# Kernel tuning notes

Measured on AMD Instinct MI355X. Metric: run time of the kernel, lower is better.

The kernel has to match this reference:

```python
import jax, jax.numpy as jnp
import numpy as np

B, V, NF, H, W, K = 16, 6890, 13776, 512, 512, 1
SIGMA = 1e-4   # BlendParams default
GAMMA = 1e-4   # BlendParams default
ZNEAR, ZFAR = 1.0, 100.0  # softmax_rgb_blend defaults (cameras not forwarded)
BG = jnp.zeros((3,), jnp.float32)  # background_color = 0.0
EPS = 1e-10


def setup_inputs() -> dict:
    key = jax.random.key(0)
    k0, k1, k2, k3, k4 = jax.random.split(key, 5)
    mesh_verts = jax.random.normal(k0, (B, V, 3), jnp.float32)
    mesh_faces = jax.random.randint(k1, (NF, 3), 0, V)
    pix_to_face = jax.random.randint(k2, (B, H, W, K), -1, NF)  # -1 = background
    zbuf = jax.random.uniform(k3, (B, H, W, K), jnp.float32, 0.0, 100.0)
    dists = jax.random.normal(k4, (B, H, W, K), jnp.float32) * SIGMA
    return {"mesh_verts": mesh_verts, "zbuf": zbuf, "dists": dists,
            "mesh_faces": mesh_faces, "pix_to_face": pix_to_face}


def _vertex_normals(verts, faces):
    # pytorch3d Meshes.verts_normals: area-weighted face normals scattered to verts
    fv = verts[:, faces]                                   # [B, F, 3(verts), 3(xyz)]
    fn = jnp.cross(fv[:, :, 1] - fv[:, :, 0], fv[:, :, 2] - fv[:, :, 0])  # [B,F,3]
    vn = jnp.zeros_like(verts)
    vn = vn.at[:, faces[:, 0]].add(fn)
    vn = vn.at[:, faces[:, 1]].add(fn)
    vn = vn.at[:, faces[:, 2]].add(fn)
    nrm = jnp.linalg.norm(vn, axis=-1, keepdims=True)
    return vn / jnp.maximum(nrm, 1e-6)                     # F.normalize(eps=1e-6)


def reference(mesh_verts, zbuf, dists, mesh_faces, pix_to_face):
    vn = _vertex_normals(mesh_verts, mesh_faces)           # [B, V, 3]
    # interpolate_face_attributes with bary = ones -> sum of the face's 3 vertex normals
    face_attr_sum = vn[:, mesh_faces].sum(axis=2)          # [B, F, 3]
    idx = jnp.clip(pix_to_face, 0, NF - 1)                 # [B, H, W, K]
    pn = jax.vmap(lambda t, i: t[i])(face_attr_sum, idx)   # [B, H, W, K, 3]
    valid = (pix_to_face >= 0)                             # [B, H, W, K]
    pn = pn * valid[..., None].astype(pn.dtype)
    # F.normalize(dim=-1), torch eps=1e-12 via clamp_min on the norm
    pn_nrm = jnp.linalg.norm(pn, axis=-1, keepdims=True)
    pixel_normals = pn / jnp.maximum(pn_nrm, 1e-12)        # [B, H, W, K, 3]

    # softmax_rgb_blend (colors = pixel_normals)
    maskf = valid.astype(jnp.float32)
    prob = jax.nn.sigmoid(-dists / SIGMA) * maskf          # [B, H, W, K]
    alpha = 1.0 - jnp.prod(1.0 - prob, axis=-1)            # [B, H, W]
    z_inv = (ZFAR - zbuf) / (ZFAR - ZNEAR) * maskf
    z_inv_max = jnp.maximum(jnp.max(z_inv, axis=-1, keepdims=True), EPS)
    weights_num = prob * jnp.exp((z_inv - z_inv_max) / GAMMA)
    delta = jnp.maximum(jnp.exp((EPS - z_inv_max) / GAMMA), EPS)
    denom = weights_num.sum(axis=-1, keepdims=True) + delta
    weighted_colors = jnp.einsum('bhwk,bhwkc->bhwc', weights_num / denom, pixel_normals)
    weighted_bg = (delta / denom) * BG                     # [B, H, W, 3]
    rendered_rgb = weighted_colors + weighted_bg
    rendered_alpha = (1.0 - alpha)[..., None]              # [B, H, W, 1]

    # faces_per_pixel == 1 path: mask from norm of (normalized) pixel normals
    hit = jnp.linalg.norm(pixel_normals, axis=-1) != 0     # [B, H, W, K]
    normalized_img = pixel_normals[:, :, :, 0, :] + (1.0 - hit[..., 0:1].astype(jnp.float32))
    out = jnp.concatenate([normalized_img, rendered_alpha], axis=-1)  # [B, H, W, 4]
    return out
```

## Files before the change

kernel.cpp:

```cpp
#include <hip/hip_runtime.h>
#include <math.h>

#define BB 16
#define VV 6890
#define NFF 13776
#define HH 512
#define WW 512

typedef float nf4 __attribute__((ext_vector_type(4)));

__global__ __launch_bounds__(256) void k_fn(const float* __restrict__ verts,
                                            const int* __restrict__ faces,
                                            float4* __restrict__ fn4) {
    int i = blockIdx.x * 256 + threadIdx.x;
    if (i >= BB * NFF) return;
    int b = i / NFF;
    int f = i - b * NFF;
    int i0 = faces[3 * f + 0];
    int i1 = faces[3 * f + 1];
    int i2 = faces[3 * f + 2];
    const float* vb = verts + (size_t)b * (VV * 3);
    float ax = vb[3 * i0 + 0], ay = vb[3 * i0 + 1], az = vb[3 * i0 + 2];
    float bx = vb[3 * i1 + 0], by = vb[3 * i1 + 1], bz = vb[3 * i1 + 2];
    float cx = vb[3 * i2 + 0], cy = vb[3 * i2 + 1], cz = vb[3 * i2 + 2];
    float e1x = bx - ax, e1y = by - ay, e1z = bz - az;
    float e2x = cx - ax, e2y = cy - ay, e2z = cz - az;
    float4 n;
    n.x = e1y * e2z - e1z * e2y;
    n.y = e1z * e2x - e1x * e2z;
    n.z = e1x * e2y - e1y * e2x;
    n.w = 0.f;
    fn4[i] = n;
}

__global__ __launch_bounds__(256) void k_count(const int* __restrict__ faces,
                                               int* __restrict__ counts) {
    int f = blockIdx.x * 256 + threadIdx.x;
    if (f >= NFF) return;
    atomicAdd(&counts[faces[3 * f + 0]], 1);
    atomicAdd(&counts[faces[3 * f + 1]], 1);
    atomicAdd(&counts[faces[3 * f + 2]], 1);
}

#define SCAN_T 1024
__global__ __launch_bounds__(SCAN_T) void k_scan(int* __restrict__ counts) {
    __shared__ int part[SCAN_T];
    const int CH = (VV + SCAN_T - 1) / SCAN_T;
    int t = threadIdx.x;
    int base = t * CH;
    int local = 0;
    for (int k = 0; k < CH; k++) {
        int idx = base + k;
        if (idx < VV) local += counts[idx];
    }
    part[t] = local;
    __syncthreads();
    for (int off = 1; off < SCAN_T; off <<= 1) {
        int v = part[t];
        int add = (t >= off) ? part[t - off] : 0;
        __syncthreads();
        part[t] = v + add;
        __syncthreads();
    }
    int running = (t == 0) ? 0 : part[t - 1];
    for (int k = 0; k < CH; k++) {
        int idx = base + k;
        if (idx < VV) {
            int c = counts[idx];
            counts[idx] = running;
            running += c;
        }
    }
    if (t == 0) counts[VV] = part[SCAN_T - 1];
}

__global__ __launch_bounds__(256) void k_fill(const int* __restrict__ faces,
                                              const int* __restrict__ offsets,
                                              int* __restrict__ cursor,
                                              int* __restrict__ adj) {
    int f = blockIdx.x * 256 + threadIdx.x;
    if (f >= NFF) return;
    for (int c = 0; c < 3; c++) {
        int v = faces[3 * f + c];
        int pos = offsets[v] + atomicAdd(&cursor[v], 1);
        adj[pos] = f;
    }
}

__global__ __launch_bounds__(256) void k_vn(const float4* __restrict__ fn4,
                                            const int* __restrict__ offsets,
                                            const int* __restrict__ adj,
                                            float4* __restrict__ vn4) {
    int i = blockIdx.x * 256 + threadIdx.x;
    if (i >= BB * VV) return;
    int b = i / VV;
    int v = i - b * VV;
    int s = offsets[v], e = offsets[v + 1];
    float x = 0.f, y = 0.f, z = 0.f;
    const float4* fnb = fn4 + (size_t)b * NFF;
    for (int j = s; j < e; j++) {
        float4 n = fnb[adj[j]];
        x += n.x; y += n.y; z += n.z;
    }
    float nrm = sqrtf(x * x + y * y + z * z);
    float inv = 1.0f / fmaxf(nrm, 1e-6f);
    float4 o; o.x = x * inv; o.y = y * inv; o.z = z * inv; o.w = 0.f;
    vn4[i] = o;
}

__global__ __launch_bounds__(256) void k_face_sum(const float4* __restrict__ vn4,
                                                  const int* __restrict__ faces,
                                                  float4* __restrict__ fas4) {
    int i = blockIdx.x * 256 + threadIdx.x;
    if (i >= BB * NFF) return;
    int b = i / NFF;
    int f = i - b * NFF;
    int i0 = faces[3 * f + 0], i1 = faces[3 * f + 1], i2 = faces[3 * f + 2];
    const float4* vnb = vn4 + (size_t)b * VV;
    float4 a = vnb[i0], bb = vnb[i1], cc = vnb[i2];
    float4 o;
    o.x = a.x + bb.x + cc.x;
    o.y = a.y + bb.y + cc.y;
    o.z = a.z + bb.z + cc.z;
    o.w = 0.f;
    fas4[i] = o;
}

__device__ __forceinline__ nf4 pixel_one(int f, float d, const float4* __restrict__ fasb) {
    float px = 0.f, py = 0.f, pz = 0.f, prob = 0.f;
    if (f >= 0) {
        int fc = f < (NFF - 1) ? f : (NFF - 1);
        float4 p = fasb[fc];
        px = p.x; py = p.y; pz = p.z;
        prob = 1.0f / (1.0f + __expf(d * 1.0e4f));
    }
    float n2 = px * px + py * py + pz * pz;
    float inv = 1.0f / fmaxf(sqrtf(n2), 1e-12f);
    float hitadd = (n2 > 0.f) ? 0.f : 1.0f;
    nf4 o;
    o.x = px * inv + hitadd;
    o.y = py * inv + hitadd;
    o.z = pz * inv + hitadd;
    o.w = 1.0f - prob;
    return o;
}

__global__ __launch_bounds__(256) void k_pixel(const int* __restrict__ p2f,
                                               const float* __restrict__ dists,
                                               const float4* __restrict__ fas4,
                                               nf4* __restrict__ out) {
    int i = (blockIdx.x * 256 + threadIdx.x) * 2;
    if (i >= BB * HH * WW) return;
    int b = i >> 18;
    int2 ff = *(const int2*)(p2f + i);
    float2 dd = *(const float2*)(dists + i);
    const float4* fasb = fas4 + (size_t)b * NFF;
    nf4 o0 = pixel_one(ff.x, dd.x, fasb);
    nf4 o1 = pixel_one(ff.y, dd.y, fasb);
    __builtin_nontemporal_store(o0, &out[i]);
    __builtin_nontemporal_store(o1, &out[i + 1]);
}

extern "C" void kernel_launch(void* const* d_in, const int* in_sizes, int n_in,
                              void* d_out, int out_size, void* d_ws, size_t ws_size,
                              hipStream_t stream) {
    const float* verts = (const float*)d_in[0];
    const float* dists = (const float*)d_in[2];
    const int* faces   = (const int*)d_in[3];
    const int* p2f     = (const int*)d_in[4];

    char* w = (char*)d_ws;
    float4* fn4  = (float4*)w;                         w += (size_t)BB * NFF * 16;
    float4* vn4  = (float4*)w;                         w += (size_t)BB * VV * 16;
    float4* fas4 = (float4*)w;                         w += (size_t)BB * NFF * 16;
    int* counts  = (int*)w;                            w += ((VV + 1) * 4 + 12) / 16 * 16;
    int* cursor  = (int*)w;                            w += (VV * 4 + 15) / 16 * 16;
    int* adj     = (int*)w;                            w += NFF * 3 * 4;

    (void)hipMemsetAsync(counts, 0, (size_t)((VV + 1) + VV) * sizeof(int) + 32, stream);

    int nbf = BB * NFF;
    int nbv = BB * VV;

    k_fn<<<(nbf + 255) / 256, 256, 0, stream>>>(verts, faces, fn4);
    k_count<<<(NFF + 255) / 256, 256, 0, stream>>>(faces, counts);
    k_scan<<<1, SCAN_T, 0, stream>>>(counts);
    k_fill<<<(NFF + 255) / 256, 256, 0, stream>>>(faces, counts, cursor, adj);
    k_vn<<<(nbv + 255) / 256, 256, 0, stream>>>(fn4, counts, adj, vn4);
    k_face_sum<<<(nbf + 255) / 256, 256, 0, stream>>>(vn4, faces, fas4);

    int npix = BB * HH * WW;
    k_pixel<<<npix / 2 / 256, 256, 0, stream>>>(p2f, dists, fas4, (nf4*)d_out);
}
```

Measured before the change: 175.5 us.

## Fuse adjacency build into one shared-memory block and widen pixel kernel

Replaces the separate face-normal, count, scan and fill kernels plus the memset with a single launch. Block 0 builds the vertex-to-face CSR adjacency in shared memory while the other blocks compute face normals, which removes several launch gaps and global atomics. The pixel kernel now handles 8 pixels per thread with vector loads, branchless masking and hardware reciprocal instructions. Block 0 serialises the whole histogram, scan and fill on one CU and could become the critical path, and rcpf is less precise than a true division.

```diff
diff --git a/kernel.cpp b/kernel.cpp
--- a/kernel.cpp
+++ b/kernel.cpp
@@ -8,82 +8,74 @@
 #define WW 512
 
 typedef float nf4 __attribute__((ext_vector_type(4)));
+typedef int   ni4 __attribute__((ext_vector_type(4)));
 
-__global__ __launch_bounds__(256) void k_fn(const float* __restrict__ verts,
-                                            const int* __restrict__ faces,
-                                            float4* __restrict__ fn4) {
-    int i = blockIdx.x * 256 + threadIdx.x;
-    if (i >= BB * NFF) return;
-    int b = i / NFF;
-    int f = i - b * NFF;
-    int i0 = faces[3 * f + 0];
-    int i1 = faces[3 * f + 1];
-    int i2 = faces[3 * f + 2];
-    const float* vb = verts + (size_t)b * (VV * 3);
-    float ax = vb[3 * i0 + 0], ay = vb[3 * i0 + 1], az = vb[3 * i0 + 2];
-    float bx = vb[3 * i1 + 0], by = vb[3 * i1 + 1], bz = vb[3 * i1 + 2];
-    float cx = vb[3 * i2 + 0], cy = vb[3 * i2 + 1], cz = vb[3 * i2 + 2];
-    float e1x = bx - ax, e1y = by - ay, e1z = bz - az;
-    float e2x = cx - ax, e2y = cy - ay, e2z = cz - az;
-    float4 n;
-    n.x = e1y * e2z - e1z * e2y;
-    n.y = e1z * e2x - e1x * e2z;
-    n.z = e1x * e2y - e1y * e2x;
-    n.w = 0.f;
-    fn4[i] = n;
-}
+#define GEOT 1024
 
-__global__ __launch_bounds__(256) void k_count(const int* __restrict__ faces,
-                                               int* __restrict__ counts) {
-    int f = blockIdx.x * 256 + threadIdx.x;
-    if (f >= NFF) return;
-    atomicAdd(&counts[faces[3 * f + 0]], 1);
-    atomicAdd(&counts[faces[3 * f + 1]], 1);
-    atomicAdd(&counts[faces[3 * f + 2]], 1);
-}
-
-#define SCAN_T 1024
-__global__ __launch_bounds__(SCAN_T) void k_scan(int* __restrict__ counts) {
-    __shared__ int part[SCAN_T];
-    const int CH = (VV + SCAN_T - 1) / SCAN_T;
-    int t = threadIdx.x;
-    int base = t * CH;
-    int local = 0;
-    for (int k = 0; k < CH; k++) {
-        int idx = base + k;
-        if (idx < VV) local += counts[idx];
-    }
-    part[t] = local;
-    __syncthreads();
-    for (int off = 1; off < SCAN_T; off <<= 1) {
-        int v = part[t];
-        int add = (t >= off) ? part[t - off] : 0;
+__global__ __launch_bounds__(GEOT) void k_geo(const float* __restrict__ verts,
+                                              const int* __restrict__ faces,
+                                              float4* __restrict__ fn4,
+                                              int* __restrict__ offsets,
+                                              int* __restrict__ adj) {
+    int blk = blockIdx.x;
+    if (blk == 0) {
+        __shared__ int hist[VV];
+        __shared__ int part[GEOT];
+        int t = threadIdx.x;
+        for (int v = t; v < VV; v += GEOT) hist[v] = 0;
         __syncthreads();
-        part[t] = v + add;
+        for (int e = t; e < NFF * 3; e += GEOT) atomicAdd(&hist[faces[e]], 1);
         __syncthreads();
-    }
-    int running = (t == 0) ? 0 : part[t - 1];
-    for (int k = 0; k < CH; k++) {
-        int idx = base + k;
-        if (idx < VV) {
-            int c = counts[idx];
-            counts[idx] = running;
-            running += c;
+        const int CH = (VV + GEOT - 1) / GEOT;
+        int base = t * CH;
+        int local = 0;
+        for (int k = 0; k < CH; k++) { int idx = base + k; if (idx < VV) local += hist[idx]; }
+        part[t] = local;
+        __syncthreads();
+        for (int off = 1; off < GEOT; off <<= 1) {
+            int v = part[t];
+            int add = (t >= off) ? part[t - off] : 0;
+            __syncthreads();
+            part[t] = v + add;
+            __syncthreads();
         }
-    }
-    if (t == 0) counts[VV] = part[SCAN_T - 1];
-}
-
-__global__ __launch_bounds__(256) void k_fill(const int* __restrict__ faces,
-                                              const int* __restrict__ offsets,
-                                              int* __restrict__ cursor,
-                                              int* __restrict__ adj) {
-    int f = blockIdx.x * 256 + threadIdx.x;
-    if (f >= NFF) return;
-    for (int c = 0; c < 3; c++) {
-        int v = faces[3 * f + c];
-        int pos = offsets[v] + atomicAdd(&cursor[v], 1);
-        adj[pos] = f;
+        int running = (t == 0) ? 0 : part[t - 1];
+        for (int k = 0; k < CH; k++) {
+            int idx = base + k;
+            if (idx < VV) {
+                int c = hist[idx];
+                hist[idx] = running;
+                offsets[idx] = running;
+                running += c;
+            }
+        }
+        if (t == 0) offsets[VV] = NFF * 3;
+        __syncthreads();
+        for (int e = t; e < NFF * 3; e += GEOT) {
+            int v = faces[e];
+            int pos = atomicAdd(&hist[v], 1);
+            adj[pos] = e / 3;
+        }
+    } else {
+        int i = (blk - 1) * GEOT + threadIdx.x;
+        if (i >= BB * NFF) return;
+        int b = i / NFF;
+        int f = i - b * NFF;
+        int i0 = faces[3 * f + 0];
+        int i1 = faces[3 * f + 1];
+        int i2 = faces[3 * f + 2];
+        const float* vb = verts + (size_t)b * (VV * 3);
+        float ax = vb[3 * i0 + 0], ay = vb[3 * i0 + 1], az = vb[3 * i0 + 2];
+        float bx = vb[3 * i1 + 0], by = vb[3 * i1 + 1], bz = vb[3 * i1 + 2];
+        float cx = vb[3 * i2 + 0], cy = vb[3 * i2 + 1], cz = vb[3 * i2 + 2];
+        float e1x = bx - ax, e1y = by - ay, e1z = bz - az;
+        float e2x = cx - ax, e2y = cy - ay, e2z = cz - az;
+        float4 n;
+        n.x = e1y * e2z - e1z * e2y;
+        n.y = e1z * e2x - e1x * e2z;
+        n.z = e1x * e2y - e1y * e2x;
+        n.w = 0.f;
+        fn4[i] = n;
     }
 }
 
@@ -102,8 +94,7 @@
         float4 n = fnb[adj[j]];
         x += n.x; y += n.y; z += n.z;
     }
-    float nrm = sqrtf(x * x + y * y + z * z);
-    float inv = 1.0f / fmaxf(nrm, 1e-6f);
+    float inv = 1.0f / fmaxf(sqrtf(x * x + y * y + z * z), 1e-6f);
     float4 o; o.x = x * inv; o.y = y * inv; o.z = z * inv; o.w = 0.f;
     vn4[i] = o;
 }
@@ -127,15 +118,13 @@
 }
 
 __device__ __forceinline__ nf4 pixel_one(int f, float d, const float4* __restrict__ fasb) {
-    float px = 0.f, py = 0.f, pz = 0.f, prob = 0.f;
-    if (f >= 0) {
-        int fc = f < (NFF - 1) ? f : (NFF - 1);
-        float4 p = fasb[fc];
-        px = p.x; py = p.y; pz = p.z;
-        prob = 1.0f / (1.0f + __expf(d * 1.0e4f));
-    }
+    int fc = f < 0 ? 0 : (f < (NFF - 1) ? f : (NFF - 1));
+    float m = (f >= 0) ? 1.0f : 0.0f;
+    float4 p = fasb[fc];
+    float px = p.x * m, py = p.y * m, pz = p.z * m;
+    float prob = m * __builtin_amdgcn_rcpf(1.0f + __expf(d * 1.0e4f));
     float n2 = px * px + py * py + pz * pz;
-    float inv = 1.0f / fmaxf(sqrtf(n2), 1e-12f);
+    float inv = __builtin_amdgcn_rcpf(fmaxf(sqrtf(n2), 1e-12f));
     float hitadd = (n2 > 0.f) ? 0.f : 1.0f;
     nf4 o;
     o.x = px * inv + hitadd;
@@ -149,16 +138,30 @@
                                                const float* __restrict__ dists,
                                                const float4* __restrict__ fas4,
                                                nf4* __restrict__ out) {
-    int i = (blockIdx.x * 256 + threadIdx.x) * 2;
+    int i = (blockIdx.x * 256 + threadIdx.x) * 8;
     if (i >= BB * HH * WW) return;
     int b = i >> 18;
-    int2 ff = *(const int2*)(p2f + i);
-    float2 dd = *(const float2*)(dists + i);
+    ni4 f0 = *(const ni4*)(p2f + i);
+    ni4 f1 = *(const ni4*)(p2f + i + 4);
+    nf4 d0 = *(const nf4*)(dists + i);
+    nf4 d1 = *(const nf4*)(dists + i + 4);
     const float4* fasb = fas4 + (size_t)b * NFF;
-    nf4 o0 = pixel_one(ff.x, dd.x, fasb);
-    nf4 o1 = pixel_one(ff.y, dd.y, fasb);
+    nf4 o0 = pixel_one(f0.x, d0.x, fasb);
+    nf4 o1 = pixel_one(f0.y, d0.y, fasb);
+    nf4 o2 = pixel_one(f0.z, d0.z, fasb);
+    nf4 o3 = pixel_one(f0.w, d0.w, fasb);
+    nf4 o4 = pixel_one(f1.x, d1.x, fasb);
+    nf4 o5 = pixel_one(f1.y, d1.y, fasb);
+    nf4 o6 = pixel_one(f1.z, d1.z, fasb);
+    nf4 o7 = pixel_one(f1.w, d1.w, fasb);
     __builtin_nontemporal_store(o0, &out[i]);
     __builtin_nontemporal_store(o1, &out[i + 1]);
+    __builtin_nontemporal_store(o2, &out[i + 2]);
+    __builtin_nontemporal_store(o3, &out[i + 3]);
+    __builtin_nontemporal_store(o4, &out[i + 4]);
+    __builtin_nontemporal_store(o5, &out[i + 5]);
+    __builtin_nontemporal_store(o6, &out[i + 6]);
+    __builtin_nontemporal_store(o7, &out[i + 7]);
 }
 
 extern "C" void kernel_launch(void* const* d_in, const int* in_sizes, int n_in,
@@ -170,25 +173,20 @@
     const int* p2f     = (const int*)d_in[4];
 
     char* w = (char*)d_ws;
-    float4* fn4  = (float4*)w;                         w += (size_t)BB * NFF * 16;
-    float4* vn4  = (float4*)w;                         w += (size_t)BB * VV * 16;
-    float4* fas4 = (float4*)w;                         w += (size_t)BB * NFF * 16;
-    int* counts  = (int*)w;                            w += ((VV + 1) * 4 + 12) / 16 * 16;
-    int* cursor  = (int*)w;                            w += (VV * 4 + 15) / 16 * 16;
-    int* adj     = (int*)w;                            w += NFF * 3 * 4;
-
-    (void)hipMemsetAsync(counts, 0, (size_t)((VV + 1) + VV) * sizeof(int) + 32, stream);
+    float4* fn4  = (float4*)w;  w += (size_t)BB * NFF * 16;
+    float4* vn4  = (float4*)w;  w += (size_t)BB * VV * 16;
+    float4* fas4 = (float4*)w;  w += (size_t)BB * NFF * 16;
+    int* offsets = (int*)w;     w += ((VV + 1) * 4 + 12) / 16 * 16;
+    int* adj     = (int*)w;     w += NFF * 3 * 4;
 
     int nbf = BB * NFF;
     int nbv = BB * VV;
 
-    k_fn<<<(nbf + 255) / 256, 256, 0, stream>>>(verts, faces, fn4);
-    k_count<<<(NFF + 255) / 256, 256, 0, stream>>>(faces, counts);
-    k_scan<<<1, SCAN_T, 0, stream>>>(counts);
-    k_fill<<<(NFF + 255) / 256, 256, 0, stream>>>(faces, counts, cursor, adj);
-    k_vn<<<(nbv + 255) / 256, 256, 0, stream>>>(fn4, counts, adj, vn4);
+    int geo_blocks = 1 + (nbf + GEOT - 1) / GEOT;
+    k_geo<<<geo_blocks, GEOT, 0, stream>>>(verts, faces, fn4, offsets, adj);
+    k_vn<<<(nbv + 255) / 256, 256, 0, stream>>>(fn4, offsets, adj, vn4);
     k_face_sum<<<(nbf + 255) / 256, 256, 0, stream>>>(vn4, faces, fas4);
 
     int npix = BB * HH * WW;
-    k_pixel<<<npix / 2 / 256, 256, 0, stream>>>(p2f, dists, fas4, (nf4*)d_out);
+    k_pixel<<<npix / 8 / 256, 256, 0, stream>>>(p2f, dists, fas4, (nf4*)d_out);
 }
```

Result: slower. 294.6 us (+67.8%).
